# Optimization experiments

Measured on AMD Instinct MI355X. Metric: run time of the kernel, lower is better.

## Reference

```python
import jax, jax.numpy as jnp
import numpy as np

N = 50000      # num_nodes
F_IN = 128     # num_features
E = 800000     # num edges (before self-loops)
H1, D1 = 8, 16 # conv1: 8 heads x 16 dims -> 128 concat
D2 = 8         # conv2: 1 head x 8 dims
NEG_SLOPE = 0.2


def setup_inputs() -> dict:
    key = jax.random.key(0)
    ks = jax.random.split(key, 16)
    s = 0.05
    return {
        "x": jax.random.normal(ks[0], (N, F_IN), jnp.float32),
        "edge_index": jax.random.randint(ks[1], (2, E), 0, N, dtype=jnp.int64),
        "W1": jax.random.normal(ks[2], (F_IN, H1 * D1), jnp.float32) * s,
        "att_src1": jax.random.normal(ks[3], (H1, D1), jnp.float32) * s,
        "att_dst1": jax.random.normal(ks[4], (H1, D1), jnp.float32) * s,
        "b1": jnp.zeros((H1 * D1,), jnp.float32),
        "W2": jax.random.normal(ks[5], (H1 * D1, D2), jnp.float32) * s,
        "att_src2": jax.random.normal(ks[6], (1, D2), jnp.float32) * s,
        "att_dst2": jax.random.normal(ks[7], (1, D2), jnp.float32) * s,
        "b2": jnp.zeros((D2,), jnp.float32),
        "fc1_w": jax.random.normal(ks[8], (N * D2, 84), jnp.float32) * 0.005,
        "fc1_b": jnp.zeros((84,), jnp.float32),
        "fc2_w": jax.random.normal(ks[9], (84, 24), jnp.float32) * s,
        "fc2_b": jnp.zeros((24,), jnp.float32),
        "fc3_w": jax.random.normal(ks[10], (24, 2), jnp.float32) * s,
        "fc3_b": jnp.zeros((2,), jnp.float32),
    }


def gat_conv(x, src, dst, W, att_src, att_dst, bias, heads, out_dim):
    """PyG GATConv: per-head linear, edge attention, scatter-softmax over
    incoming edges per target node, weighted scatter-add aggregation."""
    n = x.shape[0]
    h = (x @ W).reshape(n, heads, out_dim)            # [N,H,D]
    a_src = jnp.einsum('nhd,hd->nh', h, att_src)      # [N,H]
    a_dst = jnp.einsum('nhd,hd->nh', h, att_dst)      # [N,H]
    e = jax.nn.leaky_relu(a_src[src] + a_dst[dst], NEG_SLOPE)  # [Et,H]
    # softmax over edges grouped by destination node (stable)
    m = jax.ops.segment_max(e, dst, num_segments=n)
    p = jnp.exp(e - m[dst])
    denom = jax.ops.segment_sum(p, dst, num_segments=n)
    alpha = p / denom[dst]                            # [Et,H]
    out = jax.ops.segment_sum(alpha[:, :, None] * h[src], dst, num_segments=n)
    return out.reshape(n, heads * out_dim) + bias


def reference(x, edge_index, W1, att_src1, att_dst1, b1,
              W2, att_src2, att_dst2, b2,
              fc1_w, fc1_b, fc2_w, fc2_b, fc3_w, fc3_b):
    # add self-loops (GATConv default add_self_loops=True)
    loop = jnp.arange(N, dtype=edge_index.dtype)
    src = jnp.concatenate([edge_index[0], loop])
    dst = jnp.concatenate([edge_index[1], loop])

    h = jax.nn.elu(gat_conv(x, src, dst, W1, att_src1, att_dst1, b1, H1, D1))
    h = jax.nn.elu(gat_conv(h, src, dst, W2, att_src2, att_dst2, b2, 1, D2))

    z = h.reshape(1, N * D2)                          # batch of one graph
    z = jax.nn.elu(z @ fc1_w + fc1_b)
    z = jax.nn.elu(z @ fc2_w + fc2_b)
    z = z @ fc3_w + fc3_b
    return jax.nn.log_softmax(z, axis=1)              # [1,2]
```

## Files before the change

### kernel.cpp

```cpp
#include <hip/hip_runtime.h>
#include <math.h>

#define N_NODES 50000
#define F_IN 128
#define NE 800000
#define NH1 8
#define ND1 16
#define ND2 8
#define NEG 0.2f
#define ZLEN (N_NODES * ND2)
#define NBLK 196
#define FC1_RPB 240
#define FC1_NB 1667

typedef __attribute__((ext_vector_type(8))) short bf16x8;
typedef __attribute__((ext_vector_type(4))) float f32x4;
typedef __attribute__((ext_vector_type(2))) float f32x2;

__device__ __forceinline__ float lrelu(float v) { return v > 0.f ? v : NEG * v; }
__device__ __forceinline__ float elu1(float v)  { return v > 0.f ? v : (__expf(v) - 1.f); }

__device__ __forceinline__ unsigned short f2bf(float f) {
    union { float f; unsigned int i; } c; c.f = f;
    unsigned int u = c.i;
    return (unsigned short)((u + 0x7FFFu + ((u >> 16) & 1u)) >> 16);
}
__device__ __forceinline__ int ei_is64(const int* __restrict__ ei) {
    return ((ei[1] | ei[3] | ei[5] | ei[7]) == 0) ? 1 : 0;
}

__global__ __launch_bounds__(256) void prep_kernel(const float* __restrict__ W,
                                                   uint4* __restrict__ wbf,
                                                   int* __restrict__ counts) {
    int i = blockIdx.x * 256 + threadIdx.x;
    if (i < N_NODES) counts[i] = 1;
    if (i < 2048) {
        int col = i >> 4, kc = i & 15;
        unsigned int u[4];
        #pragma unroll
        for (int jj = 0; jj < 4; ++jj) {
            unsigned int lo = f2bf(W[(kc * 8 + 2 * jj) * 128 + col]);
            unsigned int hi = f2bf(W[(kc * 8 + 2 * jj + 1) * 128 + col]);
            u[jj] = lo | (hi << 16);
        }
        uint4 v; v.x = u[0]; v.y = u[1]; v.z = u[2]; v.w = u[3];
        wbf[col * 16 + (kc ^ (col & 15))] = v;
    }
}

__global__ void hist_kernel(const int* __restrict__ ei, int* __restrict__ counts) {
    int t = blockIdx.x * blockDim.x + threadIdx.x;
    if (t * 4 >= NE) return;
    int d0, d1, d2, d3;
    if (ei_is64(ei)) {
        const int4* p = reinterpret_cast<const int4*>(ei + 2 * NE);
        int4 a = p[t * 2];
        int4 b = p[t * 2 + 1];
        d0 = a.x; d1 = a.z; d2 = b.x; d3 = b.z;
    } else {
        int4 a = reinterpret_cast<const int4*>(ei + NE)[t];
        d0 = a.x; d1 = a.y; d2 = a.z; d3 = a.w;
    }
    atomicAdd(&counts[d0], 1);
    atomicAdd(&counts[d1], 1);
    atomicAdd(&counts[d2], 1);
    atomicAdd(&counts[d3], 1);
}

__global__ __launch_bounds__(256) void scan1_kernel(const int* __restrict__ counts,
                                                    int* __restrict__ bsum) {
    const int t = threadIdx.x;
    int i = blockIdx.x * 256 + t;
    int v = (i < N_NODES) ? counts[i] : 0;
    #pragma unroll
    for (int off = 32; off; off >>= 1) v += __shfl_down(v, off, 64);
    __shared__ int ws[4];
    if ((t & 63) == 0) ws[t >> 6] = v;
    __syncthreads();
    if (t == 0) bsum[blockIdx.x] = ws[0] + ws[1] + ws[2] + ws[3];
}

__global__ __launch_bounds__(256) void scan3_kernel(const int* __restrict__ counts,
                                                    const int* __restrict__ bsum,
                                                    int* __restrict__ rowptr,
                                                    int* __restrict__ cursor) {
    __shared__ int wsum[4];
    __shared__ int wpre[4];
    __shared__ int s_boff;
    const int t = threadIdx.x;
    const int lane = t & 63, w = t >> 6;
    int i = blockIdx.x * 256 + t;
    int v = (i < N_NODES) ? counts[i] : 0;
    int incl = v;
    #pragma unroll
    for (int off = 1; off < 64; off <<= 1) {
        int u = __shfl_up(incl, off, 64);
        if (lane >= off) incl += u;
    }
    if (lane == 63) wsum[w] = incl;
    if (t < 64) {
        int s = 0;
        for (int k = t; k < blockIdx.x; k += 64) s += bsum[k];
        #pragma unroll
        for (int off = 32; off; off >>= 1) s += __shfl_down(s, off, 64);
        if (t == 0) s_boff = s;
    }
    __syncthreads();
    if (t == 0) { int s = 0; for (int j = 0; j < 4; ++j) { wpre[j] = s; s += wsum[j]; } }
    __syncthreads();
    incl += wpre[w] + s_boff;
    if (i < N_NODES) { rowptr[i + 1] = incl; cursor[i] = incl - v; }
    if (i == 0) rowptr[0] = 0;
}

__global__ void fill_kernel(const int* __restrict__ ei,
                            int* __restrict__ cursor, int* __restrict__ esrc) {
    const int t = blockIdx.x * blockDim.x + threadIdx.x;
    const int NT_E = NE / 4;
    if (t < NT_E) {
        int s0, s1, s2, s3, d0, d1, d2, d3;
        if (ei_is64(ei)) {
            const int4* ps = reinterpret_cast<const int4*>(ei);
            const int4* pd = reinterpret_cast<const int4*>(ei + 2 * NE);
            int4 sa = ps[t * 2], sb = ps[t * 2 + 1];
            int4 da = pd[t * 2], db = pd[t * 2 + 1];
            s0 = sa.x; s1 = sa.z; s2 = sb.x; s3 = sb.z;
            d0 = da.x; d1 = da.z; d2 = db.x; d3 = db.z;
        } else {
            int4 sa = reinterpret_cast<const int4*>(ei)[t];
            int4 da = reinterpret_cast<const int4*>(ei + NE)[t];
            s0 = sa.x; s1 = sa.y; s2 = sa.z; s3 = sa.w;
            d0 = da.x; d1 = da.y; d2 = da.z; d3 = da.w;
        }
        esrc[atomicAdd(&cursor[d0], 1)] = s0;
        esrc[atomicAdd(&cursor[d1], 1)] = s1;
        esrc[atomicAdd(&cursor[d2], 1)] = s2;
        esrc[atomicAdd(&cursor[d3], 1)] = s3;
    } else {
        int i = t - NT_E;
        if (i < N_NODES) esrc[atomicAdd(&cursor[i], 1)] = i;
    }
}

__global__ __launch_bounds__(256) void gemm1_kernel(const float* __restrict__ x,
                                                    const uint4* __restrict__ wbf,
                                                    const float* __restrict__ att_src,
                                                    const float* __restrict__ att_dst,
                                                    unsigned int* __restrict__ h1f8,
                                                    float* __restrict__ a_src1,
                                                    float* __restrict__ a_dst1) {
    __shared__ uint4 Xs[1024];
    __shared__ uint4 Ws[2048];
    const int t = threadIdx.x;
    const int row0 = blockIdx.x * 64;

    #pragma unroll
    for (int p = 0; p < 8; ++p) Ws[p * 256 + t] = wbf[p * 256 + t];

    #pragma unroll
    for (int p = 0; p < 4; ++p) {
        int cidx = p * 256 + t;
        int row = cidx >> 4, c = cidx & 15;
        int grow = row0 + row;
        float4 xa = make_float4(0.f, 0.f, 0.f, 0.f);
        float4 xb = make_float4(0.f, 0.f, 0.f, 0.f);
        if (grow < N_NODES) {
            xa = *reinterpret_cast<const float4*>(x + (size_t)grow * F_IN + c * 8);
            xb = *reinterpret_cast<const float4*>(x + (size_t)grow * F_IN + c * 8 + 4);
        }
        uint4 u;
        u.x = (unsigned int)f2bf(xa.x) | ((unsigned int)f2bf(xa.y) << 16);
        u.y = (unsigned int)f2bf(xa.z) | ((unsigned int)f2bf(xa.w) << 16);
        u.z = (unsigned int)f2bf(xb.x) | ((unsigned int)f2bf(xb.y) << 16);
        u.w = (unsigned int)f2bf(xb.z) | ((unsigned int)f2bf(xb.w) << 16);
        Xs[row * 16 + (c ^ (row & 15))] = u;
    }
    __syncthreads();

    const int wv = t >> 6;
    const int l  = t & 63;
    const int d  = l & 15;
    const int g  = l >> 4;
    const int arow = wv * 16 + d;

    f32x4 acc[8];
    #pragma unroll
    for (int n = 0; n < 8; ++n) { acc[n][0] = 0.f; acc[n][1] = 0.f; acc[n][2] = 0.f; acc[n][3] = 0.f; }

    #pragma unroll
    for (int ks = 0; ks < 4; ++ks) {
        int kc = ks * 4 + g;
        union { uint4 u; bf16x8 v; } A;
        A.u = Xs[arow * 16 + (kc ^ d)];
        #pragma unroll
        for (int n = 0; n < 8; ++n) {
            union { uint4 u; bf16x8 v; } B;
            B.u = Ws[(n * 16 + d) * 16 + (kc ^ d)];
            acc[n] = __builtin_amdgcn_mfma_f32_16x16x32_bf16(A.v, B.v, acc[n], 0, 0, 0);
        }
    }

    float as8[8], ad8[8];
    #pragma unroll
    for (int n = 0; n < 8; ++n) { as8[n] = att_src[n * 16 + d]; ad8[n] = att_dst[n * 16 + d]; }
    #pragma unroll
    for (int n = 0; n < 8; ++n) {
        #pragma unroll
        for (int r = 0; r < 4; ++r) {
            float ps = acc[n][r] * as8[n];
            float pd = acc[n][r] * ad8[n];
            #pragma unroll
            for (int off = 1; off < 16; off <<= 1) {
                ps += __shfl_xor(ps, off, 16);
                pd += __shfl_xor(pd, off, 16);
            }
            int grow = row0 + wv * 16 + g * 4 + r;
            if (d == 0 && grow < N_NODES) {
                a_src1[grow * 8 + n] = ps;
                a_dst1[grow * 8 + n] = pd;
            }
        }
    }
    #pragma unroll
    for (int n = 0; n < 8; ++n) {
        #pragma unroll
        for (int r = 0; r < 4; ++r) {
            float v = acc[n][r];
            float v1 = __shfl_xor(v, 1, 64);
            int p01 = __builtin_amdgcn_cvt_pk_fp8_f32(v, v1, 0, false);
            int p23 = __shfl_xor(p01, 2, 64);
            int grow = row0 + wv * 16 + g * 4 + r;
            if (((d & 3) == 0) && grow < N_NODES) {
                unsigned int u = ((unsigned int)p01 & 0xFFFFu) | ((unsigned int)p23 << 16);
                h1f8[(size_t)grow * 32 + n * 4 + (d >> 2)] = u;
            }
        }
    }
}

__global__ __launch_bounds__(256) void agg1_kernel(const unsigned int* __restrict__ h1f8,
                                                   const float* __restrict__ a_src,
                                                   const float* __restrict__ a_dst,
                                                   const int* __restrict__ rowptr,
                                                   const int* __restrict__ esrc,
                                                   const float* __restrict__ b1,
                                                   float* __restrict__ hout) {
    int wid = (blockIdx.x * 256 + threadIdx.x) >> 6;
    if (wid >= N_NODES) return;
    const int lane = threadIdx.x & 63;
    const int m    = lane & 31;
    const int half = lane >> 5;
    const int h    = m >> 2;
    const float ad = a_dst[wid * 8 + h];
    float a0 = 0.f, a1 = 0.f, a2 = 0.f, a3 = 0.f, den = 0.f;
    int j = rowptr[wid];
    const int jend = rowptr[wid + 1];
    for (; j + 8 <= jend; j += 8) {
        int s[4];
        #pragma unroll
        for (int k = 0; k < 4; ++k) s[k] = esrc[j + 2 * k + half];
        unsigned int u[4];
        #pragma unroll
        for (int k = 0; k < 4; ++k) u[k] = h1f8[(size_t)s[k] * 32 + m];
        float e[4];
        #pragma unroll
        for (int k = 0; k < 4; ++k) e[k] = a_src[s[k] * 8 + h];
        #pragma unroll
        for (int k = 0; k < 4; ++k) {
            float p = __expf(lrelu(e[k] + ad));
            den += p;
            f32x2 lo = __builtin_amdgcn_cvt_pk_f32_fp8(u[k], false);
            f32x2 hi = __builtin_amdgcn_cvt_pk_f32_fp8(u[k], true);
            a0 = fmaf(p, lo[0], a0); a1 = fmaf(p, lo[1], a1);
            a2 = fmaf(p, hi[0], a2); a3 = fmaf(p, hi[1], a3);
        }
    }
    for (; j < jend; j += 2) {
        int e_idx = j + half;
        if (e_idx < jend) {
            int s = esrc[e_idx];
            unsigned int u = h1f8[(size_t)s * 32 + m];
            float e = a_src[s * 8 + h];
            float p = __expf(lrelu(e + ad));
            den += p;
            f32x2 lo = __builtin_amdgcn_cvt_pk_f32_fp8(u, false);
            f32x2 hi = __builtin_amdgcn_cvt_pk_f32_fp8(u, true);
            a0 = fmaf(p, lo[0], a0); a1 = fmaf(p, lo[1], a1);
            a2 = fmaf(p, hi[0], a2); a3 = fmaf(p, hi[1], a3);
        }
    }
    a0  += __shfl_xor(a0, 32, 64);
    a1  += __shfl_xor(a1, 32, 64);
    a2  += __shfl_xor(a2, 32, 64);
    a3  += __shfl_xor(a3, 32, 64);
    den += __shfl_xor(den, 32, 64);
    if (half == 0) {
        float inv = 1.f / den;
        float4 bb = *reinterpret_cast<const float4*>(b1 + 4 * m);
        float4 o = make_float4(elu1(a0 * inv + bb.x), elu1(a1 * inv + bb.y),
                               elu1(a2 * inv + bb.z), elu1(a3 * inv + bb.w));
        *reinterpret_cast<float4*>(hout + (size_t)wid * F_IN + 4 * m) = o;
    }
}

__global__ __launch_bounds__(256) void gemm2_kernel(const float* __restrict__ h,
                                                    const float* __restrict__ W2,
                                                    const float* __restrict__ att_src2,
                                                    const float* __restrict__ att_dst2,
                                                    float* __restrict__ h2,
                                                    float* __restrict__ a_src2,
                                                    float* __restrict__ a_dst2) {
    __shared__ float Ws[F_IN * ND2];
    __shared__ float Hs[32 * 132];
    int t = threadIdx.x;
    int node0 = blockIdx.x * 32;
    #pragma unroll
    for (int i = 0; i < 4; ++i) { int idx = i * 256 + t; Ws[idx] = W2[idx]; }
    #pragma unroll
    for (int i = 0; i < 4; ++i) {
        int fidx = i * 256 + t;
        int r = fidx >> 5;
        int c4 = fidx & 31;
        int grow = node0 + r;
        float4 v = make_float4(0.f, 0.f, 0.f, 0.f);
        if (grow < N_NODES) v = *reinterpret_cast<const float4*>(h + (size_t)grow * F_IN + c4 * 4);
        *reinterpret_cast<float4*>(&Hs[r * 132 + c4 * 4]) = v;
    }
    __syncthreads();
    int nsub = t >> 3, d = t & 7;
    int node = node0 + nsub;
    float acc = 0.f;
    #pragma unroll 8
    for (int k = 0; k < F_IN; ++k)
        acc = fmaf(Hs[nsub * 132 + k], Ws[k * ND2 + d], acc);
    float vs = acc * att_src2[d];
    float vd = acc * att_dst2[d];
    #pragma unroll
    for (int off = 4; off >= 1; off >>= 1) {
        vs += __shfl_xor(vs, off, 8);
        vd += __shfl_xor(vd, off, 8);
    }
    if (node < N_NODES) {
        h2[node * ND2 + d] = acc;
        if (d == 0) { a_src2[node] = vs; a_dst2[node] = vd; }
    }
}

__global__ void agg2_kernel(const float* __restrict__ h2,
                            const float* __restrict__ a_src2, const float* __restrict__ a_dst2,
                            const int* __restrict__ rowptr, const int* __restrict__ esrc,
                            const float* __restrict__ b2, float* __restrict__ g) {
    int n = blockIdx.x * blockDim.x + threadIdx.x;
    if (n >= N_NODES) return;
    float ad = a_dst2[n];
    float acc[8] = {0.f, 0.f, 0.f, 0.f, 0.f, 0.f, 0.f, 0.f};
    float den = 0.f;
    int jend = rowptr[n + 1];
    for (int j = rowptr[n]; j < jend; ++j) {
        int s = esrc[j];
        float p = __expf(lrelu(a_src2[s] + ad));
        den += p;
        float4 va = *reinterpret_cast<const float4*>(h2 + s * ND2);
        float4 vb = *reinterpret_cast<const float4*>(h2 + s * ND2 + 4);
        acc[0] = fmaf(p, va.x, acc[0]); acc[1] = fmaf(p, va.y, acc[1]);
        acc[2] = fmaf(p, va.z, acc[2]); acc[3] = fmaf(p, va.w, acc[3]);
        acc[4] = fmaf(p, vb.x, acc[4]); acc[5] = fmaf(p, vb.y, acc[5]);
        acc[6] = fmaf(p, vb.z, acc[6]); acc[7] = fmaf(p, vb.w, acc[7]);
    }
    float inv = 1.f / den;
    float4 o0 = make_float4(elu1(acc[0] * inv + b2[0]), elu1(acc[1] * inv + b2[1]),
                            elu1(acc[2] * inv + b2[2]), elu1(acc[3] * inv + b2[3]));
    float4 o1 = make_float4(elu1(acc[4] * inv + b2[4]), elu1(acc[5] * inv + b2[5]),
                            elu1(acc[6] * inv + b2[6]), elu1(acc[7] * inv + b2[7]));
    *reinterpret_cast<float4*>(g + n * ND2)     = o0;
    *reinterpret_cast<float4*>(g + n * ND2 + 4) = o1;
}

__global__ __launch_bounds__(256) void fc1_stage1(const float* __restrict__ z,
                                                  const float* __restrict__ w,
                                                  float* __restrict__ partial) {
    __shared__ float zs[FC1_RPB];
    __shared__ float4 red[252];
    const int t = threadIdx.x;
    const int b = blockIdx.x;
    const int r0 = b * FC1_RPB;
    if (t < FC1_RPB) {
        int gr = r0 + t;
        zs[t] = (gr < ZLEN) ? z[gr] : 0.f;
    }
    __syncthreads();
    const int c4 = t % 21;
    const int rr = t / 21;
    if (t < 252) {
        float4 a = make_float4(0.f, 0.f, 0.f, 0.f);
        const float4* __restrict__ w4 = reinterpret_cast<const float4*>(w);
        if (r0 + FC1_RPB <= ZLEN) {
            #pragma unroll
            for (int bq = 0; bq < 5; ++bq) {
                float4 wv[4];
                float  zv[4];
                #pragma unroll
                for (int u = 0; u < 4; ++u) {
                    int i = bq * 48 + u * 12 + rr;
                    wv[u] = w4[(size_t)(r0 + i) * 21 + c4];
                    zv[u] = zs[i];
                }
                #pragma unroll
                for (int u = 0; u < 4; ++u) {
                    a.x = fmaf(zv[u], wv[u].x, a.x);
                    a.y = fmaf(zv[u], wv[u].y, a.y);
                    a.z = fmaf(zv[u], wv[u].z, a.z);
                    a.w = fmaf(zv[u], wv[u].w, a.w);
                }
            }
        } else {
            for (int i = rr; i < FC1_RPB; i += 12) {
                if (r0 + i < ZLEN) {
                    float4 wv = w4[(size_t)(r0 + i) * 21 + c4];
                    float  zv = zs[i];
                    a.x = fmaf(zv, wv.x, a.x); a.y = fmaf(zv, wv.y, a.y);
                    a.z = fmaf(zv, wv.z, a.z); a.w = fmaf(zv, wv.w, a.w);
                }
            }
        }
        red[t] = a;
    }
    __syncthreads();
    if (t < 21) {
        float4 s = red[t];
        #pragma unroll
        for (int k = 1; k < 12; ++k) {
            float4 v = red[k * 21 + t];
            s.x += v.x; s.y += v.y; s.z += v.z; s.w += v.w;
        }
        *reinterpret_cast<float4*>(partial + (size_t)b * 88 + t * 4) = s;
    }
}

__global__ __launch_bounds__(1024) void fctail_kernel(const float* __restrict__ partial,
                                                      const float* __restrict__ fc1_b,
                                                      const float* __restrict__ fc2_w,
                                                      const float* __restrict__ fc2_b,
                                                      const float* __restrict__ fc3_w,
                                                      const float* __restrict__ fc3_b,
                                                      float* __restrict__ out) {
    __shared__ float red[1008];
    __shared__ float z1[84];
    __shared__ float z2[24];
    const int t = threadIdx.x;
    if (t < 1008) {
        const int j  = t % 84;
        const int sl = t / 84;
        float s = 0.f;
        for (int b = sl; b < FC1_NB; b += 12)
            s += partial[(size_t)b * 88 + j];
        red[t] = s;
    }
    __syncthreads();
    if (t < 84) {
        float s = 0.f;
        #pragma unroll
        for (int sl = 0; sl < 12; ++sl) s += red[sl * 84 + t];
        z1[t] = elu1(s + fc1_b[t]);
    }
    __syncthreads();
    if (t < 24) {
        float a = fc2_b[t];
        for (int i = 0; i < 84; ++i) a = fmaf(z1[i], fc2_w[i * 24 + t], a);
        z2[t] = elu1(a);
    }
    __syncthreads();
    if (t == 0) {
        float z3[2];
        #pragma unroll
        for (int jj = 0; jj < 2; ++jj) {
            float a = fc3_b[jj];
            for (int i = 0; i < 24; ++i) a = fmaf(z2[i], fc3_w[i * 2 + jj], a);
            z3[jj] = a;
        }
        float m = fmaxf(z3[0], z3[1]);
        float l = m + logf(__expf(z3[0] - m) + __expf(z3[1] - m));
        out[0] = z3[0] - l;
        out[1] = z3[1] - l;
    }
}

extern "C" void kernel_launch(void* const* d_in, const int* in_sizes, int n_in,
                              void* d_out, int out_size, void* d_ws, size_t ws_size,
                              hipStream_t stream) {
    const float* x        = (const float*)d_in[0];
    const int*   ei       = (const int*)d_in[1];
    const float* W1       = (const float*)d_in[2];
    const float* att_src1 = (const float*)d_in[3];
    const float* att_dst1 = (const float*)d_in[4];
    const float* b1       = (const float*)d_in[5];
    const float* W2       = (const float*)d_in[6];
    const float* att_src2 = (const float*)d_in[7];
    const float* att_dst2 = (const float*)d_in[8];
    const float* b2       = (const float*)d_in[9];
    const float* fc1_w    = (const float*)d_in[10];
    const float* fc1_b    = (const float*)d_in[11];
    const float* fc2_w    = (const float*)d_in[12];
    const float* fc2_b    = (const float*)d_in[13];
    const float* fc3_w    = (const float*)d_in[14];
    const float* fc3_b    = (const float*)d_in[15];
    float* out = (float*)d_out;

    char* ws = (char*)d_ws;
    unsigned int* h1f8 = (unsigned int*)(ws + 0);
    float* hbuf   = (float*)(ws + 6400000);
    float* a_src1 = (float*)(ws + 32000000);
    float* a_dst1 = (float*)(ws + 33600000);
    float* h2     = (float*)(ws + 35200000);
    float* a_src2 = (float*)(ws + 36800000);
    float* a_dst2 = (float*)(ws + 37000000);
    float* g      = (float*)(ws + 37200000);
    int*   counts = (int*)  (ws + 38800000);
    int*   rowptr = (int*)  (ws + 39000000);
    int*   cursor = (int*)  (ws + 39200064);
    int*   esrc   = (int*)  (ws + 39400064);
    float* partial= (float*)(ws + 42800064);
    uint4* wbf    = (uint4*)(ws + 43386848);
    int*   bsum   = (int*)  (ws + 43419616);

    prep_kernel<<<NBLK, 256, 0, stream>>>(W1, wbf, counts);
    hist_kernel<<<(NE / 4 + 255) / 256, 256, 0, stream>>>(ei, counts);
    scan1_kernel<<<NBLK, 256, 0, stream>>>(counts, bsum);
    scan3_kernel<<<NBLK, 256, 0, stream>>>(counts, bsum, rowptr, cursor);
    fill_kernel<<<(NE / 4 + N_NODES + 255) / 256, 256, 0, stream>>>(ei, cursor, esrc);

    gemm1_kernel<<<(N_NODES + 63) / 64, 256, 0, stream>>>(x, wbf, att_src1, att_dst1, h1f8, a_src1, a_dst1);
    agg1_kernel<<<(N_NODES + 3) / 4, 256, 0, stream>>>(h1f8, a_src1, a_dst1, rowptr, esrc, b1, hbuf);

    gemm2_kernel<<<(N_NODES + 31) / 32, 256, 0, stream>>>(hbuf, W2, att_src2, att_dst2, h2, a_src2, a_dst2);
    agg2_kernel<<<(N_NODES + 255) / 256, 256, 0, stream>>>(h2, a_src2, a_dst2, rowptr, esrc, b2, g);

    fc1_stage1<<<FC1_NB, 256, 0, stream>>>(g, fc1_w, partial);
    fctail_kernel<<<1, 1024, 0, stream>>>(partial, fc1_b, fc2_w, fc2_b, fc3_w, fc3_b, out);
}
```

Baseline: 243.2 us.

## Fuse CSR build and conv2 stages into persistent kernels with grid barriers

Merges the histogram, two scan passes and fill kernels into one 196-block persistent kernel that separates phases with atomic-counter grid barriers and keeps edge indices in registers between the count and fill phases. Fuses gemm2 and agg2 the same way, with each block handling 256 nodes per phase. This removes several kernel launches and a second read of the edge list. In exchange the code now relies on all 196 blocks being resident at once, and the spin barriers plus reduced parallelism in the fused phases could cost time.

```diff
diff --git a/kernel.cpp b/kernel.cpp
--- a/kernel.cpp
+++ b/kernel.cpp
@@ -29,11 +29,23 @@
     return ((ei[1] | ei[3] | ei[5] | ei[7]) == 0) ? 1 : 0;
 }
 
+__device__ __forceinline__ void grid_barrier(int* cnt, int target) {
+    __threadfence();
+    __syncthreads();
+    if (threadIdx.x == 0) {
+        atomicAdd(cnt, 1);
+        while (atomicAdd(cnt, 0) < target) __builtin_amdgcn_s_sleep(8);
+    }
+    __syncthreads();
+}
+
 __global__ __launch_bounds__(256) void prep_kernel(const float* __restrict__ W,
                                                    uint4* __restrict__ wbf,
-                                                   int* __restrict__ counts) {
+                                                   int* __restrict__ counts,
+                                                   int* __restrict__ bars) {
     int i = blockIdx.x * 256 + threadIdx.x;
     if (i < N_NODES) counts[i] = 1;
+    if (i < 2) bars[i] = 0;
     if (i < 2048) {
         int col = i >> 4, kc = i & 15;
         unsigned int u[4];
@@ -48,98 +60,98 @@
     }
 }
 
-__global__ void hist_kernel(const int* __restrict__ ei, int* __restrict__ counts) {
-    int t = blockIdx.x * blockDim.x + threadIdx.x;
-    if (t * 4 >= NE) return;
-    int d0, d1, d2, d3;
-    if (ei_is64(ei)) {
-        const int4* p = reinterpret_cast<const int4*>(ei + 2 * NE);
-        int4 a = p[t * 2];
-        int4 b = p[t * 2 + 1];
-        d0 = a.x; d1 = a.z; d2 = b.x; d3 = b.z;
-    } else {
-        int4 a = reinterpret_cast<const int4*>(ei + NE)[t];
-        d0 = a.x; d1 = a.y; d2 = a.z; d3 = a.w;
-    }
-    atomicAdd(&counts[d0], 1);
-    atomicAdd(&counts[d1], 1);
-    atomicAdd(&counts[d2], 1);
-    atomicAdd(&counts[d3], 1);
-}
-
-__global__ __launch_bounds__(256) void scan1_kernel(const int* __restrict__ counts,
-                                                    int* __restrict__ bsum) {
-    const int t = threadIdx.x;
-    int i = blockIdx.x * 256 + t;
-    int v = (i < N_NODES) ? counts[i] : 0;
-    #pragma unroll
-    for (int off = 32; off; off >>= 1) v += __shfl_down(v, off, 64);
-    __shared__ int ws[4];
-    if ((t & 63) == 0) ws[t >> 6] = v;
-    __syncthreads();
-    if (t == 0) bsum[blockIdx.x] = ws[0] + ws[1] + ws[2] + ws[3];
-}
-
-__global__ __launch_bounds__(256) void scan3_kernel(const int* __restrict__ counts,
-                                                    const int* __restrict__ bsum,
-                                                    int* __restrict__ rowptr,
-                                                    int* __restrict__ cursor) {
+__global__ __launch_bounds__(256) void csr_kernel(const int* __restrict__ ei,
+                                                  int* __restrict__ counts,
+                                                  int* __restrict__ bsum,
+                                                  int* __restrict__ rowptr,
+                                                  int* __restrict__ cursor,
+                                                  int* __restrict__ esrc,
+                                                  int* __restrict__ bar) {
     __shared__ int wsum[4];
     __shared__ int wpre[4];
     __shared__ int s_boff;
     const int t = threadIdx.x;
-    const int lane = t & 63, w = t >> 6;
-    int i = blockIdx.x * 256 + t;
-    int v = (i < N_NODES) ? counts[i] : 0;
-    int incl = v;
-    #pragma unroll
-    for (int off = 1; off < 64; off <<= 1) {
-        int u = __shfl_up(incl, off, 64);
-        if (lane >= off) incl += u;
-    }
-    if (lane == 63) wsum[w] = incl;
-    if (t < 64) {
-        int s = 0;
-        for (int k = t; k < blockIdx.x; k += 64) s += bsum[k];
-        #pragma unroll
-        for (int off = 32; off; off >>= 1) s += __shfl_down(s, off, 64);
-        if (t == 0) s_boff = s;
-    }
-    __syncthreads();
-    if (t == 0) { int s = 0; for (int j = 0; j < 4; ++j) { wpre[j] = s; s += wsum[j]; } }
-    __syncthreads();
-    incl += wpre[w] + s_boff;
-    if (i < N_NODES) { rowptr[i + 1] = incl; cursor[i] = incl - v; }
-    if (i == 0) rowptr[0] = 0;
-}
-
-__global__ void fill_kernel(const int* __restrict__ ei,
-                            int* __restrict__ cursor, int* __restrict__ esrc) {
-    const int t = blockIdx.x * blockDim.x + threadIdx.x;
-    const int NT_E = NE / 4;
-    if (t < NT_E) {
-        int s0, s1, s2, s3, d0, d1, d2, d3;
-        if (ei_is64(ei)) {
-            const int4* ps = reinterpret_cast<const int4*>(ei);
-            const int4* pd = reinterpret_cast<const int4*>(ei + 2 * NE);
-            int4 sa = ps[t * 2], sb = ps[t * 2 + 1];
-            int4 da = pd[t * 2], db = pd[t * 2 + 1];
-            s0 = sa.x; s1 = sa.z; s2 = sb.x; s3 = sb.z;
-            d0 = da.x; d1 = da.z; d2 = db.x; d3 = db.z;
-        } else {
-            int4 sa = reinterpret_cast<const int4*>(ei)[t];
-            int4 da = reinterpret_cast<const int4*>(ei + NE)[t];
-            s0 = sa.x; s1 = sa.y; s2 = sa.z; s3 = sa.w;
-            d0 = da.x; d1 = da.y; d2 = da.z; d3 = da.w;
-        }
-        esrc[atomicAdd(&cursor[d0], 1)] = s0;
-        esrc[atomicAdd(&cursor[d1], 1)] = s1;
-        esrc[atomicAdd(&cursor[d2], 1)] = s2;
-        esrc[atomicAdd(&cursor[d3], 1)] = s3;
-    } else {
-        int i = t - NT_E;
-        if (i < N_NODES) esrc[atomicAdd(&cursor[i], 1)] = i;
-    }
+    const int b = blockIdx.x;
+    const int gtid = b * 256 + t;
+    const int nthr = NBLK * 256;
+    const int NQ = NE / 4;
+    const int is64 = ei_is64(ei);
+
+    int4 sq[4], dq[4];
+    int nq = 0;
+    #pragma unroll
+    for (int k = 0; k < 4; ++k) {
+        int q = gtid + k * nthr;
+        if (q < NQ) {
+            int4 s4, d4;
+            if (is64) {
+                const int4* ps = reinterpret_cast<const int4*>(ei);
+                const int4* pd = reinterpret_cast<const int4*>(ei + 2 * NE);
+                int4 sa = ps[q * 2], sb = ps[q * 2 + 1];
+                int4 da = pd[q * 2], db = pd[q * 2 + 1];
+                s4 = make_int4(sa.x, sa.z, sb.x, sb.z);
+                d4 = make_int4(da.x, da.z, db.x, db.z);
+            } else {
+                s4 = reinterpret_cast<const int4*>(ei)[q];
+                d4 = reinterpret_cast<const int4*>(ei + NE)[q];
+            }
+            sq[k] = s4; dq[k] = d4;
+            atomicAdd(&counts[d4.x], 1);
+            atomicAdd(&counts[d4.y], 1);
+            atomicAdd(&counts[d4.z], 1);
+            atomicAdd(&counts[d4.w], 1);
+            nq = k + 1;
+        }
+    }
+    grid_barrier(bar, NBLK);
+
+    {
+        int v = (gtid < N_NODES) ? counts[gtid] : 0;
+        int r = v;
+        #pragma unroll
+        for (int off = 32; off; off >>= 1) r += __shfl_down(r, off, 64);
+        if ((t & 63) == 0) wsum[t >> 6] = r;
+        __syncthreads();
+        if (t == 0) bsum[b] = wsum[0] + wsum[1] + wsum[2] + wsum[3];
+    }
+    grid_barrier(bar, NBLK * 2);
+
+    {
+        const int lane = t & 63, w = t >> 6;
+        int v = (gtid < N_NODES) ? counts[gtid] : 0;
+        int incl = v;
+        #pragma unroll
+        for (int off = 1; off < 64; off <<= 1) {
+            int u = __shfl_up(incl, off, 64);
+            if (lane >= off) incl += u;
+        }
+        if (lane == 63) wsum[w] = incl;
+        if (t < 64) {
+            int s = 0;
+            for (int k = t; k < b; k += 64) s += bsum[k];
+            #pragma unroll
+            for (int off = 32; off; off >>= 1) s += __shfl_down(s, off, 64);
+            if (t == 0) s_boff = s;
+        }
+        __syncthreads();
+        if (t == 0) { int s = 0; for (int j = 0; j < 4; ++j) { wpre[j] = s; s += wsum[j]; } }
+        __syncthreads();
+        incl += wpre[w] + s_boff;
+        if (gtid < N_NODES) { rowptr[gtid + 1] = incl; cursor[gtid] = incl - v; }
+        if (gtid == 0) rowptr[0] = 0;
+    }
+    grid_barrier(bar, NBLK * 3);
+
+    #pragma unroll
+    for (int k = 0; k < 4; ++k) {
+        if (k < nq) {
+            esrc[atomicAdd(&cursor[dq[k].x], 1)] = sq[k].x;
+            esrc[atomicAdd(&cursor[dq[k].y], 1)] = sq[k].y;
+            esrc[atomicAdd(&cursor[dq[k].z], 1)] = sq[k].z;
+            esrc[atomicAdd(&cursor[dq[k].w], 1)] = sq[k].w;
+        }
+    }
+    if (gtid < N_NODES) esrc[atomicAdd(&cursor[gtid], 1)] = gtid;
 }
 
 __global__ __launch_bounds__(256) void gemm1_kernel(const float* __restrict__ x,
@@ -303,77 +315,83 @@
     }
 }
 
-__global__ __launch_bounds__(256) void gemm2_kernel(const float* __restrict__ h,
+__global__ __launch_bounds__(256) void conv2_kernel(const float* __restrict__ h,
                                                     const float* __restrict__ W2,
                                                     const float* __restrict__ att_src2,
                                                     const float* __restrict__ att_dst2,
+                                                    const int* __restrict__ rowptr,
+                                                    const int* __restrict__ esrc,
+                                                    const float* __restrict__ b2,
                                                     float* __restrict__ h2,
                                                     float* __restrict__ a_src2,
-                                                    float* __restrict__ a_dst2) {
+                                                    float* __restrict__ a_dst2,
+                                                    float* __restrict__ g,
+                                                    int* __restrict__ bar) {
     __shared__ float Ws[F_IN * ND2];
     __shared__ float Hs[32 * 132];
-    int t = threadIdx.x;
-    int node0 = blockIdx.x * 32;
+    const int t = threadIdx.x;
     #pragma unroll
     for (int i = 0; i < 4; ++i) { int idx = i * 256 + t; Ws[idx] = W2[idx]; }
-    #pragma unroll
-    for (int i = 0; i < 4; ++i) {
-        int fidx = i * 256 + t;
-        int r = fidx >> 5;
-        int c4 = fidx & 31;
-        int grow = node0 + r;
-        float4 v = make_float4(0.f, 0.f, 0.f, 0.f);
-        if (grow < N_NODES) v = *reinterpret_cast<const float4*>(h + (size_t)grow * F_IN + c4 * 4);
-        *reinterpret_cast<float4*>(&Hs[r * 132 + c4 * 4]) = v;
-    }
-    __syncthreads();
-    int nsub = t >> 3, d = t & 7;
-    int node = node0 + nsub;
-    float acc = 0.f;
-    #pragma unroll 8
-    for (int k = 0; k < F_IN; ++k)
-        acc = fmaf(Hs[nsub * 132 + k], Ws[k * ND2 + d], acc);
-    float vs = acc * att_src2[d];
-    float vd = acc * att_dst2[d];
-    #pragma unroll
-    for (int off = 4; off >= 1; off >>= 1) {
-        vs += __shfl_xor(vs, off, 8);
-        vd += __shfl_xor(vd, off, 8);
-    }
-    if (node < N_NODES) {
-        h2[node * ND2 + d] = acc;
-        if (d == 0) { a_src2[node] = vs; a_dst2[node] = vd; }
-    }
-}
-
-__global__ void agg2_kernel(const float* __restrict__ h2,
-                            const float* __restrict__ a_src2, const float* __restrict__ a_dst2,
-                            const int* __restrict__ rowptr, const int* __restrict__ esrc,
-                            const float* __restrict__ b2, float* __restrict__ g) {
-    int n = blockIdx.x * blockDim.x + threadIdx.x;
-    if (n >= N_NODES) return;
-    float ad = a_dst2[n];
-    float acc[8] = {0.f, 0.f, 0.f, 0.f, 0.f, 0.f, 0.f, 0.f};
-    float den = 0.f;
-    int jend = rowptr[n + 1];
-    for (int j = rowptr[n]; j < jend; ++j) {
-        int s = esrc[j];
-        float p = __expf(lrelu(a_src2[s] + ad));
-        den += p;
-        float4 va = *reinterpret_cast<const float4*>(h2 + s * ND2);
-        float4 vb = *reinterpret_cast<const float4*>(h2 + s * ND2 + 4);
-        acc[0] = fmaf(p, va.x, acc[0]); acc[1] = fmaf(p, va.y, acc[1]);
-        acc[2] = fmaf(p, va.z, acc[2]); acc[3] = fmaf(p, va.w, acc[3]);
-        acc[4] = fmaf(p, vb.x, acc[4]); acc[5] = fmaf(p, vb.y, acc[5]);
-        acc[6] = fmaf(p, vb.z, acc[6]); acc[7] = fmaf(p, vb.w, acc[7]);
-    }
-    float inv = 1.f / den;
-    float4 o0 = make_float4(elu1(acc[0] * inv + b2[0]), elu1(acc[1] * inv + b2[1]),
-                            elu1(acc[2] * inv + b2[2]), elu1(acc[3] * inv + b2[3]));
-    float4 o1 = make_float4(elu1(acc[4] * inv + b2[4]), elu1(acc[5] * inv + b2[5]),
-                            elu1(acc[6] * inv + b2[6]), elu1(acc[7] * inv + b2[7]));
-    *reinterpret_cast<float4*>(g + n * ND2)     = o0;
-    *reinterpret_cast<float4*>(g + n * ND2 + 4) = o1;
+
+    for (int sub = 0; sub < 8; ++sub) {
+        int node0 = (blockIdx.x * 8 + sub) * 32;
+        __syncthreads();
+        #pragma unroll
+        for (int i = 0; i < 4; ++i) {
+            int fidx = i * 256 + t;
+            int r = fidx >> 5;
+            int c4 = fidx & 31;
+            int grow = node0 + r;
+            float4 v = make_float4(0.f, 0.f, 0.f, 0.f);
+            if (grow < N_NODES) v = *reinterpret_cast<const float4*>(h + (size_t)grow * F_IN + c4 * 4);
+            *reinterpret_cast<float4*>(&Hs[r * 132 + c4 * 4]) = v;
+        }
+        __syncthreads();
+        int nsub = t >> 3, d = t & 7;
+        int node = node0 + nsub;
+        float acc = 0.f;
+        #pragma unroll 8
+        for (int k = 0; k < F_IN; ++k)
+            acc = fmaf(Hs[nsub * 132 + k], Ws[k * ND2 + d], acc);
+        float vs = acc * att_src2[d];
+        float vd = acc * att_dst2[d];
+        #pragma unroll
+        for (int off = 4; off >= 1; off >>= 1) {
+            vs += __shfl_xor(vs, off, 8);
+            vd += __shfl_xor(vd, off, 8);
+        }
+        if (node < N_NODES) {
+            h2[node * ND2 + d] = acc;
+            if (d == 0) { a_src2[node] = vs; a_dst2[node] = vd; }
+        }
+    }
+    grid_barrier(bar, NBLK);
+
+    int n = blockIdx.x * 256 + t;
+    if (n < N_NODES) {
+        float ad = a_dst2[n];
+        float acc[8] = {0.f, 0.f, 0.f, 0.f, 0.f, 0.f, 0.f, 0.f};
+        float den = 0.f;
+        int jend = rowptr[n + 1];
+        for (int j = rowptr[n]; j < jend; ++j) {
+            int s = esrc[j];
+            float p = __expf(lrelu(a_src2[s] + ad));
+            den += p;
+            float4 va = *reinterpret_cast<const float4*>(h2 + s * ND2);
+            float4 vb = *reinterpret_cast<const float4*>(h2 + s * ND2 + 4);
+            acc[0] = fmaf(p, va.x, acc[0]); acc[1] = fmaf(p, va.y, acc[1]);
+            acc[2] = fmaf(p, va.z, acc[2]); acc[3] = fmaf(p, va.w, acc[3]);
+            acc[4] = fmaf(p, vb.x, acc[4]); acc[5] = fmaf(p, vb.y, acc[5]);
+            acc[6] = fmaf(p, vb.z, acc[6]); acc[7] = fmaf(p, vb.w, acc[7]);
+        }
+        float inv = 1.f / den;
+        float4 o0 = make_float4(elu1(acc[0] * inv + b2[0]), elu1(acc[1] * inv + b2[1]),
+                                elu1(acc[2] * inv + b2[2]), elu1(acc[3] * inv + b2[3]));
+        float4 o1 = make_float4(elu1(acc[4] * inv + b2[4]), elu1(acc[5] * inv + b2[5]),
+                                elu1(acc[6] * inv + b2[6]), elu1(acc[7] * inv + b2[7]));
+        *reinterpret_cast<float4*>(g + n * ND2)     = o0;
+        *reinterpret_cast<float4*>(g + n * ND2 + 4) = o1;
+    }
 }
 
 __global__ __launch_bounds__(256) void fc1_stage1(const float* __restrict__ z,
@@ -522,18 +540,16 @@
     float* partial= (float*)(ws + 42800064);
     uint4* wbf    = (uint4*)(ws + 43386848);
     int*   bsum   = (int*)  (ws + 43419616);
-
-    prep_kernel<<<NBLK, 256, 0, stream>>>(W1, wbf, counts);
-    hist_kernel<<<(NE / 4 + 255) / 256, 256, 0, stream>>>(ei, counts);
-    scan1_kernel<<<NBLK, 256, 0, stream>>>(counts, bsum);
-    scan3_kernel<<<NBLK, 256, 0, stream>>>(counts, bsum, rowptr, cursor);
-    fill_kernel<<<(NE / 4 + N_NODES + 255) / 256, 256, 0, stream>>>(ei, cursor, esrc);
+    int*   bars   = (int*)  (ws + 43420416);
+
+    prep_kernel<<<NBLK, 256, 0, stream>>>(W1, wbf, counts, bars);
+    csr_kernel<<<NBLK, 256, 0, stream>>>(ei, counts, bsum, rowptr, cursor, esrc, &bars[0]);
 
     gemm1_kernel<<<(N_NODES + 63) / 64, 256, 0, stream>>>(x, wbf, att_src1, att_dst1, h1f8, a_src1, a_dst1);
     agg1_kernel<<<(N_NODES + 3) / 4, 256, 0, stream>>>(h1f8, a_src1, a_dst1, rowptr, esrc, b1, hbuf);
 
-    gemm2_kernel<<<(N_NODES + 31) / 32, 256, 0, stream>>>(hbuf, W2, att_src2, att_dst2, h2, a_src2, a_dst2);
-    agg2_kernel<<<(N_NODES + 255) / 256, 256, 0, stream>>>(h2, a_src2, a_dst2, rowptr, esrc, b2, g);
+    conv2_kernel<<<NBLK, 256, 0, stream>>>(hbuf, W2, att_src2, att_dst2, rowptr, esrc, b2,
+                                           h2, a_src2, a_dst2, g, &bars[1]);
 
     fc1_stage1<<<FC1_NB, 256, 0, stream>>>(g, fc1_w, partial);
     fctail_kernel<<<1, 1024, 0, stream>>>(partial, fc1_b, fc2_w, fc2_b, fc3_w, fc3_b, out);
```

Result: slower. 313.7 us (+29.0%).

## Cut kernel launches: fuse scans, fold W1 prep into gemm1, grid-barrier conv2

Applied to the files above, without the earlier changes.

Drops prep_kernel: W1 is now converted to bf16 inside each gemm1 block, and counts is zeroed with a memset while the self-loop +1 moves into the scan. The two scan kernels become one single-pass scan that uses per-block flags and a decoupled lookback. gemm2 and agg2 are merged into one persistent conv2 kernel of 196 blocks separated by a software grid barrier. The aim is fewer launches and less inter-kernel gap time, at the cost of redundant W1 conversion per block, reduced parallelism in conv2's gemm phase, and reliance on all blocks being co-resident. The flag and barrier buffers are cleared by the memset.

```diff
diff --git a/kernel.cpp b/kernel.cpp
--- a/kernel.cpp
+++ b/kernel.cpp
@@ -29,23 +29,15 @@
     return ((ei[1] | ei[3] | ei[5] | ei[7]) == 0) ? 1 : 0;
 }
 
-__global__ __launch_bounds__(256) void prep_kernel(const float* __restrict__ W,
-                                                   uint4* __restrict__ wbf,
-                                                   int* __restrict__ counts) {
-    int i = blockIdx.x * 256 + threadIdx.x;
-    if (i < N_NODES) counts[i] = 1;
-    if (i < 2048) {
-        int col = i >> 4, kc = i & 15;
-        unsigned int u[4];
-        #pragma unroll
-        for (int jj = 0; jj < 4; ++jj) {
-            unsigned int lo = f2bf(W[(kc * 8 + 2 * jj) * 128 + col]);
-            unsigned int hi = f2bf(W[(kc * 8 + 2 * jj + 1) * 128 + col]);
-            u[jj] = lo | (hi << 16);
-        }
-        uint4 v; v.x = u[0]; v.y = u[1]; v.z = u[2]; v.w = u[3];
-        wbf[col * 16 + (kc ^ (col & 15))] = v;
-    }
+__device__ __forceinline__ void grid_barrier(int* cnt, int target) {
+    __threadfence();
+    __syncthreads();
+    if (threadIdx.x == 0) {
+        atomicAdd(cnt, 1);
+        while (atomicAdd(cnt, 0) < target) __builtin_amdgcn_s_sleep(8);
+        __threadfence();
+    }
+    __syncthreads();
 }
 
 __global__ void hist_kernel(const int* __restrict__ ei, int* __restrict__ counts) {
@@ -67,30 +59,19 @@
     atomicAdd(&counts[d3], 1);
 }
 
-__global__ __launch_bounds__(256) void scan1_kernel(const int* __restrict__ counts,
-                                                    int* __restrict__ bsum) {
-    const int t = threadIdx.x;
-    int i = blockIdx.x * 256 + t;
-    int v = (i < N_NODES) ? counts[i] : 0;
-    #pragma unroll
-    for (int off = 32; off; off >>= 1) v += __shfl_down(v, off, 64);
-    __shared__ int ws[4];
-    if ((t & 63) == 0) ws[t >> 6] = v;
-    __syncthreads();
-    if (t == 0) bsum[blockIdx.x] = ws[0] + ws[1] + ws[2] + ws[3];
-}
-
-__global__ __launch_bounds__(256) void scan3_kernel(const int* __restrict__ counts,
-                                                    const int* __restrict__ bsum,
-                                                    int* __restrict__ rowptr,
-                                                    int* __restrict__ cursor) {
+__global__ __launch_bounds__(256) void scan_kernel(const int* __restrict__ counts,
+                                                   int* __restrict__ bsum,
+                                                   int* __restrict__ flag,
+                                                   int* __restrict__ rowptr,
+                                                   int* __restrict__ cursor) {
     __shared__ int wsum[4];
     __shared__ int wpre[4];
     __shared__ int s_boff;
     const int t = threadIdx.x;
+    const int b = blockIdx.x;
     const int lane = t & 63, w = t >> 6;
-    int i = blockIdx.x * 256 + t;
-    int v = (i < N_NODES) ? counts[i] : 0;
+    const int i = b * 256 + t;
+    int v = (i < N_NODES) ? counts[i] + 1 : 0;
     int incl = v;
     #pragma unroll
     for (int off = 1; off < 64; off <<= 1) {
@@ -98,15 +79,26 @@
         if (lane >= off) incl += u;
     }
     if (lane == 63) wsum[w] = incl;
-    if (t < 64) {
+    __syncthreads();
+    if (t == 0) {
         int s = 0;
-        for (int k = t; k < blockIdx.x; k += 64) s += bsum[k];
+        #pragma unroll
+        for (int j = 0; j < 4; ++j) { wpre[j] = s; s += wsum[j]; }
+        bsum[b] = s;
+        __threadfence();
+        atomicExch(&flag[b], 1);
+    }
+    if (t >= 64 && t < 128) {
+        int tl = t - 64;
+        int s = 0;
+        for (int k = tl; k < b; k += 64) {
+            while (atomicAdd(&flag[k], 0) == 0) __builtin_amdgcn_s_sleep(2);
+            s += atomicAdd(&bsum[k], 0);
+        }
         #pragma unroll
         for (int off = 32; off; off >>= 1) s += __shfl_down(s, off, 64);
-        if (t == 0) s_boff = s;
-    }
-    __syncthreads();
-    if (t == 0) { int s = 0; for (int j = 0; j < 4; ++j) { wpre[j] = s; s += wsum[j]; } }
+        if (tl == 0) s_boff = s;
+    }
     __syncthreads();
     incl += wpre[w] + s_boff;
     if (i < N_NODES) { rowptr[i + 1] = incl; cursor[i] = incl - v; }
@@ -143,7 +135,7 @@
 }
 
 __global__ __launch_bounds__(256) void gemm1_kernel(const float* __restrict__ x,
-                                                    const uint4* __restrict__ wbf,
+                                                    const float* __restrict__ W1,
                                                     const float* __restrict__ att_src,
                                                     const float* __restrict__ att_dst,
                                                     unsigned int* __restrict__ h1f8,
@@ -155,7 +147,19 @@
     const int row0 = blockIdx.x * 64;
 
     #pragma unroll
-    for (int p = 0; p < 8; ++p) Ws[p * 256 + t] = wbf[p * 256 + t];
+    for (int p = 0; p < 8; ++p) {
+        int idx = p * 256 + t;
+        int col = idx >> 4, kc = idx & 15;
+        unsigned int uu[4];
+        #pragma unroll
+        for (int jj = 0; jj < 4; ++jj) {
+            unsigned int lo = f2bf(W1[(kc * 8 + 2 * jj) * 128 + col]);
+            unsigned int hi = f2bf(W1[(kc * 8 + 2 * jj + 1) * 128 + col]);
+            uu[jj] = lo | (hi << 16);
+        }
+        uint4 vv; vv.x = uu[0]; vv.y = uu[1]; vv.z = uu[2]; vv.w = uu[3];
+        Ws[col * 16 + (kc ^ (col & 15))] = vv;
+    }
 
     #pragma unroll
     for (int p = 0; p < 4; ++p) {
@@ -303,77 +307,83 @@
     }
 }
 
-__global__ __launch_bounds__(256) void gemm2_kernel(const float* __restrict__ h,
+__global__ __launch_bounds__(256) void conv2_kernel(const float* __restrict__ h,
                                                     const float* __restrict__ W2,
                                                     const float* __restrict__ att_src2,
                                                     const float* __restrict__ att_dst2,
+                                                    const int* __restrict__ rowptr,
+                                                    const int* __restrict__ esrc,
+                                                    const float* __restrict__ b2,
                                                     float* __restrict__ h2,
                                                     float* __restrict__ a_src2,
-                                                    float* __restrict__ a_dst2) {
+                                                    float* __restrict__ a_dst2,
+                                                    float* __restrict__ g,
+                                                    int* __restrict__ bar) {
     __shared__ float Ws[F_IN * ND2];
     __shared__ float Hs[32 * 132];
-    int t = threadIdx.x;
-    int node0 = blockIdx.x * 32;
+    const int t = threadIdx.x;
     #pragma unroll
     for (int i = 0; i < 4; ++i) { int idx = i * 256 + t; Ws[idx] = W2[idx]; }
-    #pragma unroll
-    for (int i = 0; i < 4; ++i) {
-        int fidx = i * 256 + t;
-        int r = fidx >> 5;
-        int c4 = fidx & 31;
-        int grow = node0 + r;
-        float4 v = make_float4(0.f, 0.f, 0.f, 0.f);
-        if (grow < N_NODES) v = *reinterpret_cast<const float4*>(h + (size_t)grow * F_IN + c4 * 4);
-        *reinterpret_cast<float4*>(&Hs[r * 132 + c4 * 4]) = v;
-    }
-    __syncthreads();
-    int nsub = t >> 3, d = t & 7;
-    int node = node0 + nsub;
-    float acc = 0.f;
-    #pragma unroll 8
-    for (int k = 0; k < F_IN; ++k)
-        acc = fmaf(Hs[nsub * 132 + k], Ws[k * ND2 + d], acc);
-    float vs = acc * att_src2[d];
-    float vd = acc * att_dst2[d];
-    #pragma unroll
-    for (int off = 4; off >= 1; off >>= 1) {
-        vs += __shfl_xor(vs, off, 8);
-        vd += __shfl_xor(vd, off, 8);
-    }
-    if (node < N_NODES) {
-        h2[node * ND2 + d] = acc;
-        if (d == 0) { a_src2[node] = vs; a_dst2[node] = vd; }
-    }
-}
-
-__global__ void agg2_kernel(const float* __restrict__ h2,
-                            const float* __restrict__ a_src2, const float* __restrict__ a_dst2,
-                            const int* __restrict__ rowptr, const int* __restrict__ esrc,
-                            const float* __restrict__ b2, float* __restrict__ g) {
-    int n = blockIdx.x * blockDim.x + threadIdx.x;
-    if (n >= N_NODES) return;
-    float ad = a_dst2[n];
-    float acc[8] = {0.f, 0.f, 0.f, 0.f, 0.f, 0.f, 0.f, 0.f};
-    float den = 0.f;
-    int jend = rowptr[n + 1];
-    for (int j = rowptr[n]; j < jend; ++j) {
-        int s = esrc[j];
-        float p = __expf(lrelu(a_src2[s] + ad));
-        den += p;
-        float4 va = *reinterpret_cast<const float4*>(h2 + s * ND2);
-        float4 vb = *reinterpret_cast<const float4*>(h2 + s * ND2 + 4);
-        acc[0] = fmaf(p, va.x, acc[0]); acc[1] = fmaf(p, va.y, acc[1]);
-        acc[2] = fmaf(p, va.z, acc[2]); acc[3] = fmaf(p, va.w, acc[3]);
-        acc[4] = fmaf(p, vb.x, acc[4]); acc[5] = fmaf(p, vb.y, acc[5]);
-        acc[6] = fmaf(p, vb.z, acc[6]); acc[7] = fmaf(p, vb.w, acc[7]);
-    }
-    float inv = 1.f / den;
-    float4 o0 = make_float4(elu1(acc[0] * inv + b2[0]), elu1(acc[1] * inv + b2[1]),
-                            elu1(acc[2] * inv + b2[2]), elu1(acc[3] * inv + b2[3]));
-    float4 o1 = make_float4(elu1(acc[4] * inv + b2[4]), elu1(acc[5] * inv + b2[5]),
-                            elu1(acc[6] * inv + b2[6]), elu1(acc[7] * inv + b2[7]));
-    *reinterpret_cast<float4*>(g + n * ND2)     = o0;
-    *reinterpret_cast<float4*>(g + n * ND2 + 4) = o1;
+
+    for (int sub = 0; sub < 8; ++sub) {
+        int node0 = (blockIdx.x * 8 + sub) * 32;
+        __syncthreads();
+        #pragma unroll
+        for (int i = 0; i < 4; ++i) {
+            int fidx = i * 256 + t;
+            int r = fidx >> 5;
+            int c4 = fidx & 31;
+            int grow = node0 + r;
+            float4 v = make_float4(0.f, 0.f, 0.f, 0.f);
+            if (grow < N_NODES) v = *reinterpret_cast<const float4*>(h + (size_t)grow * F_IN + c4 * 4);
+            *reinterpret_cast<float4*>(&Hs[r * 132 + c4 * 4]) = v;
+        }
+        __syncthreads();
+        int nsub = t >> 3, d = t & 7;
+        int node = node0 + nsub;
+        float acc = 0.f;
+        #pragma unroll 8
+        for (int k = 0; k < F_IN; ++k)
+            acc = fmaf(Hs[nsub * 132 + k], Ws[k * ND2 + d], acc);
+        float vs = acc * att_src2[d];
+        float vd = acc * att_dst2[d];
+        #pragma unroll
+        for (int off = 4; off >= 1; off >>= 1) {
+            vs += __shfl_xor(vs, off, 8);
+            vd += __shfl_xor(vd, off, 8);
+        }
+        if (node < N_NODES) {
+            h2[node * ND2 + d] = acc;
+            if (d == 0) { a_src2[node] = vs; a_dst2[node] = vd; }
+        }
+    }
+    grid_barrier(bar, NBLK);
+
+    int n = blockIdx.x * 256 + t;
+    if (n < N_NODES) {
+        float ad = a_dst2[n];
+        float acc[8] = {0.f, 0.f, 0.f, 0.f, 0.f, 0.f, 0.f, 0.f};
+        float den = 0.f;
+        int jend = rowptr[n + 1];
+        for (int j = rowptr[n]; j < jend; ++j) {
+            int s = esrc[j];
+            float p = __expf(lrelu(a_src2[s] + ad));
+            den += p;
+            float4 va = *reinterpret_cast<const float4*>(h2 + s * ND2);
+            float4 vb = *reinterpret_cast<const float4*>(h2 + s * ND2 + 4);
+            acc[0] = fmaf(p, va.x, acc[0]); acc[1] = fmaf(p, va.y, acc[1]);
+            acc[2] = fmaf(p, va.z, acc[2]); acc[3] = fmaf(p, va.w, acc[3]);
+            acc[4] = fmaf(p, vb.x, acc[4]); acc[5] = fmaf(p, vb.y, acc[5]);
+            acc[6] = fmaf(p, vb.z, acc[6]); acc[7] = fmaf(p, vb.w, acc[7]);
+        }
+        float inv = 1.f / den;
+        float4 o0 = make_float4(elu1(acc[0] * inv + b2[0]), elu1(acc[1] * inv + b2[1]),
+                                elu1(acc[2] * inv + b2[2]), elu1(acc[3] * inv + b2[3]));
+        float4 o1 = make_float4(elu1(acc[4] * inv + b2[4]), elu1(acc[5] * inv + b2[5]),
+                                elu1(acc[6] * inv + b2[6]), elu1(acc[7] * inv + b2[7]));
+        *reinterpret_cast<float4*>(g + n * ND2)     = o0;
+        *reinterpret_cast<float4*>(g + n * ND2 + 4) = o1;
+    }
 }
 
 __global__ __launch_bounds__(256) void fc1_stage1(const float* __restrict__ z,
@@ -516,24 +526,25 @@
     float* a_dst2 = (float*)(ws + 37000000);
     float* g      = (float*)(ws + 37200000);
     int*   counts = (int*)  (ws + 38800000);
-    int*   rowptr = (int*)  (ws + 39000000);
-    int*   cursor = (int*)  (ws + 39200064);
-    int*   esrc   = (int*)  (ws + 39400064);
-    float* partial= (float*)(ws + 42800064);
-    uint4* wbf    = (uint4*)(ws + 43386848);
-    int*   bsum   = (int*)  (ws + 43419616);
-
-    prep_kernel<<<NBLK, 256, 0, stream>>>(W1, wbf, counts);
+    int*   flag   = (int*)  (ws + 39000000);
+    int*   bars   = (int*)  (ws + 39000784);
+    int*   rowptr = (int*)  (ws + 39000800);
+    int*   cursor = (int*)  (ws + 39200864);
+    int*   esrc   = (int*)  (ws + 39400864);
+    float* partial= (float*)(ws + 42800864);
+    int*   bsum   = (int*)  (ws + 43387648);
+
+    hipMemsetAsync(counts, 0, 200800, stream);
+
     hist_kernel<<<(NE / 4 + 255) / 256, 256, 0, stream>>>(ei, counts);
-    scan1_kernel<<<NBLK, 256, 0, stream>>>(counts, bsum);
-    scan3_kernel<<<NBLK, 256, 0, stream>>>(counts, bsum, rowptr, cursor);
+    scan_kernel<<<NBLK, 256, 0, stream>>>(counts, bsum, flag, rowptr, cursor);
     fill_kernel<<<(NE / 4 + N_NODES + 255) / 256, 256, 0, stream>>>(ei, cursor, esrc);
 
-    gemm1_kernel<<<(N_NODES + 63) / 64, 256, 0, stream>>>(x, wbf, att_src1, att_dst1, h1f8, a_src1, a_dst1);
+    gemm1_kernel<<<(N_NODES + 63) / 64, 256, 0, stream>>>(x, W1, att_src1, att_dst1, h1f8, a_src1, a_dst1);
     agg1_kernel<<<(N_NODES + 3) / 4, 256, 0, stream>>>(h1f8, a_src1, a_dst1, rowptr, esrc, b1, hbuf);
 
-    gemm2_kernel<<<(N_NODES + 31) / 32, 256, 0, stream>>>(hbuf, W2, att_src2, att_dst2, h2, a_src2, a_dst2);
-    agg2_kernel<<<(N_NODES + 255) / 256, 256, 0, stream>>>(h2, a_src2, a_dst2, rowptr, esrc, b2, g);
+    conv2_kernel<<<NBLK, 256, 0, stream>>>(hbuf, W2, att_src2, att_dst2, rowptr, esrc, b2,
+                                           h2, a_src2, a_dst2, g, &bars[0]);
 
     fc1_stage1<<<FC1_NB, 256, 0, stream>>>(g, fc1_w, partial);
     fctail_kernel<<<1, 1024, 0, stream>>>(partial, fc1_b, fc2_w, fc2_b, fc3_w, fc3_b, out);
```

Measured after the change: 301.5 us. 1.24x slower.
